# Kernel tuning notes

Hardware: AMD Instinct MI355X
Metric: run time of the kernel (lower is better)

The kernel has to match this reference:

```python
import jax, jax.numpy as jnp
import numpy as np

N_NODES = 100000
N_EDGES = 1_600_000
IN_CH = 64
HID = 128
OUT_CH = 2


def _glorot(key, shape):
    fan_in = shape[0]
    return jax.random.normal(key, shape, dtype=jnp.float32) / jnp.sqrt(jnp.float32(fan_in))


def setup_inputs() -> dict:
    key = jax.random.key(0)
    ks = jax.random.split(key, 10)
    x = jax.random.normal(ks[0], (N_NODES, IN_CH), dtype=jnp.float32)
    edge_index = jax.random.randint(ks[1], (2, N_EDGES), 0, N_NODES, dtype=jnp.int64)
    # SAGEConv layer 0: lin_l (neighbor, with bias) + lin_r (root)
    W_n0 = _glorot(ks[2], (IN_CH, HID))
    W_s0 = _glorot(ks[3], (IN_CH, HID))
    b0 = jnp.zeros((HID,), dtype=jnp.float32)
    # SAGEConv layer 1
    W_n1 = _glorot(ks[4], (HID, HID))
    W_s1 = _glorot(ks[5], (HID, HID))
    b1 = jnp.zeros((HID,), dtype=jnp.float32)
    # final fc
    fc_w = _glorot(ks[6], (HID, OUT_CH))
    fc_b = jnp.zeros((OUT_CH,), dtype=jnp.float32)
    return {"x": x, "edge_index": edge_index, "W_n0": W_n0, "W_s0": W_s0, "b0": b0,
            "W_n1": W_n1, "W_s1": W_s1, "b1": b1, "fc_w": fc_w, "fc_b": fc_b}


def _sage_conv(h, src, dst, W_n, W_s, b, num_nodes):
    # mean aggregation of source features onto destination nodes
    agg = jax.ops.segment_sum(h[src], dst, num_segments=num_nodes)  # [N, d]
    cnt = jax.ops.segment_sum(jnp.ones_like(dst, dtype=h.dtype), dst, num_segments=num_nodes)
    mean = agg / jnp.maximum(cnt, 1.0)[:, None]
    return mean @ W_n + h @ W_s + b


def reference(x, edge_index, W_n0, W_s0, b0, W_n1, W_s1, b1, fc_w, fc_b):
    src, dst = edge_index[0], edge_index[1]
    n = x.shape[0]
    h = jax.nn.relu(_sage_conv(x, src, dst, W_n0, W_s0, b0, n))  # dropout is identity in eval mode
    h = jax.nn.relu(_sage_conv(h, src, dst, W_n1, W_s1, b1, n))
    return h @ fc_w + fc_b
```

## Files before the change

kernel.cpp:

```cpp
#include <hip/hip_runtime.h>

#define N_NODES 100000
#define IN_CH 64
#define HID 128
#define NBUCK ((N_NODES + 511) >> 9)
#define NCB 256

typedef short short8 __attribute__((ext_vector_type(8)));
typedef float floatx4 __attribute__((ext_vector_type(4)));
typedef float floatx2 __attribute__((ext_vector_type(2)));

__device__ __forceinline__ unsigned short f2bf(float f) {
    unsigned u = __builtin_bit_cast(unsigned, f);
    u += 0x7fffu + ((u >> 16) & 1u);
    return (unsigned short)(u >> 16);
}

template <int K>
__device__ __forceinline__ void pack_dev(const float* __restrict__ Wn,
                                         const float* __restrict__ Ws,
                                         unsigned short* __restrict__ Bpack, int idx) {
    int s = idx >> 9;
    int rem = idx & 511;
    int t = rem >> 6;
    int lane = rem & 63;
    int quad = lane >> 4;
    int n = t * 16 + (lane & 15);
    unsigned short v[8];
#pragma unroll
    for (int j = 0; j < 8; ++j) {
        int k = s * 32 + quad * 8 + j;
        float w = (k < K) ? Wn[(size_t)k * HID + n] : Ws[(size_t)(k - K) * HID + n];
        v[j] = f2bf(w);
    }
    *(short8*)(Bpack + (size_t)idx * 8) = *(short8*)v;
}

__global__ __launch_bounds__(256) void histprep_kernel(const int* __restrict__ dst,
                                                       int* __restrict__ table, int E, int chunk,
                                                       const float* __restrict__ x,
                                                       unsigned short* __restrict__ x_bf,
                                                       unsigned char* __restrict__ x_f8,
                                                       const float* __restrict__ Wn0,
                                                       const float* __restrict__ Ws0,
                                                       unsigned short* __restrict__ Bpack0,
                                                       const float* __restrict__ Wn1,
                                                       const float* __restrict__ Ws1,
                                                       unsigned short* __restrict__ Bpack1,
                                                       int* __restrict__ scan_done, int n4) {
    int b = blockIdx.x;
    if (b < NCB) {
        if (b == 0 && threadIdx.x == 0) *scan_done = 0;
        __shared__ int h[NBUCK];
        for (int i = threadIdx.x; i < NBUCK; i += 256) h[i] = 0;
        __syncthreads();
        int e0 = b * chunk;
        int e1 = min(E, e0 + chunk);
        for (int e = e0 + threadIdx.x; e < e1; e += 256) atomicAdd(&h[dst[e] >> 9], 1);
        __syncthreads();
        for (int i = threadIdx.x; i < NBUCK; i += 256) table[i * NCB + b] = h[i];
    } else if (b < NCB + 8) {
        pack_dev<IN_CH>(Wn0, Ws0, Bpack0, (b - NCB) * 256 + threadIdx.x);
    } else if (b < NCB + 24) {
        pack_dev<HID>(Wn1, Ws1, Bpack1, (b - NCB - 8) * 256 + threadIdx.x);
    } else {
        int i = (b - NCB - 24) * 256 + threadIdx.x;
        if (i < n4) {
            float4 v = ((const float4*)x)[i];
            ushort4 o;
            o.x = f2bf(v.x); o.y = f2bf(v.y); o.z = f2bf(v.z); o.w = f2bf(v.w);
            ((ushort4*)x_bf)[i] = o;
            int p8 = __builtin_amdgcn_cvt_pk_fp8_f32(v.x, v.y, 0, false);
            p8 = __builtin_amdgcn_cvt_pk_fp8_f32(v.z, v.w, p8, true);
            ((unsigned*)x_f8)[i] = (unsigned)p8;
        }
    }
}

__global__ __launch_bounds__(256) void scan12_kernel(int* __restrict__ table,
                                                     int* __restrict__ tot,
                                                     int* __restrict__ bstart,
                                                     int* __restrict__ ptr,
                                                     int* __restrict__ scan_done, int E) {
    __shared__ int s[NCB];
    __shared__ int lastflag;
    int b = blockIdx.x, t = threadIdx.x;
    int c = table[b * NCB + t];
    s[t] = c;
    __syncthreads();
#pragma unroll
    for (int off = 1; off < NCB; off <<= 1) {
        int v = (t >= off) ? s[t - off] : 0;
        __syncthreads();
        s[t] += v;
        __syncthreads();
    }
    table[b * NCB + t] = s[t] - c;
    if (t == NCB - 1) {
        __hip_atomic_store(&tot[b], s[t], __ATOMIC_RELAXED, __HIP_MEMORY_SCOPE_AGENT);
        int prev = __hip_atomic_fetch_add(scan_done, 1, __ATOMIC_ACQ_REL, __HIP_MEMORY_SCOPE_AGENT);
        lastflag = (prev == NBUCK - 1);
    }
    __syncthreads();
    if (!lastflag) return;
    int v = (t < NBUCK) ? __hip_atomic_load(&tot[t], __ATOMIC_RELAXED, __HIP_MEMORY_SCOPE_AGENT) : 0;
    s[t] = v;
    __syncthreads();
#pragma unroll
    for (int off = 1; off < 256; off <<= 1) {
        int u = (t >= off) ? s[t - off] : 0;
        __syncthreads();
        s[t] += u;
        __syncthreads();
    }
    if (t < NBUCK) bstart[t] = s[t] - v;
    if (t == 0) {
        bstart[NBUCK] = E;
        ptr[N_NODES] = E;
    }
}

__global__ __launch_bounds__(256) void bin_kernel(const int* __restrict__ src,
                                                  const int* __restrict__ dst,
                                                  const int* __restrict__ table,
                                                  const int* __restrict__ bstart,
                                                  unsigned* __restrict__ binned, int E, int chunk) {
    __shared__ int cur[NBUCK];
    int blk = blockIdx.x;
    for (int i = threadIdx.x; i < NBUCK; i += 256) cur[i] = bstart[i] + table[i * NCB + blk];
    __syncthreads();
    int e0 = blk * chunk;
    int e1 = min(E, e0 + chunk);
    for (int e = e0 + threadIdx.x; e < e1; e += 256) {
        int d = dst[e];
        int b = d >> 9;
        int pos = atomicAdd(&cur[b], 1);
        binned[pos] = (unsigned)src[e] | ((unsigned)(d & 511) << 17);
    }
}

__global__ __launch_bounds__(256) void place_kernel(const unsigned* __restrict__ binned,
                                                    const int* __restrict__ bstart,
                                                    int* __restrict__ ptr,
                                                    int* __restrict__ sorted, int N) {
    __shared__ int deg[512];
    __shared__ int cur[512];
    __shared__ int ssum[256];
    int b = blockIdx.x, t = threadIdx.x;
    int start = bstart[b], end = bstart[b + 1];
    deg[t] = 0;
    deg[t + 256] = 0;
    __syncthreads();
    for (int i = start + t; i < end; i += 256) atomicAdd(&deg[binned[i] >> 17], 1);
    __syncthreads();
    int a = deg[2 * t], c = deg[2 * t + 1];
    int s2 = a + c;
    ssum[t] = s2;
    __syncthreads();
#pragma unroll
    for (int off = 1; off < 256; off <<= 1) {
        int u = (t >= off) ? ssum[t - off] : 0;
        __syncthreads();
        ssum[t] += u;
        __syncthreads();
    }
    int excl2 = ssum[t] - s2;
    cur[2 * t] = excl2;
    cur[2 * t + 1] = excl2 + a;
    int n0 = b * 512 + 2 * t;
    if (n0 < N) ptr[n0] = start + excl2;
    if (n0 + 1 < N) ptr[n0 + 1] = start + excl2 + a;
    __syncthreads();
    for (int i = start + t; i < end; i += 256) {
        unsigned p = binned[i];
        int dl = p >> 17;
        int pos = start + atomicAdd(&cur[dl], 1);
        sorted[pos] = (int)(p & 0x1FFFF);
    }
}

template <int C>
__global__ __launch_bounds__(256) void gather_mean_f8(const int* __restrict__ ptr,
                                                      const int* __restrict__ srcs,
                                                      const unsigned char* __restrict__ feat,
                                                      unsigned short* __restrict__ mean, int N) {
    constexpr int NA = C / 64;
    int w = (blockIdx.x * blockDim.x + threadIdx.x) >> 6;
    if (w >= N) return;
    int lane = threadIdx.x & 63;
    int g = lane >> 4;
    int l = lane & 15;
    int s0 = ptr[w], s1 = ptr[w + 1];
    int deg = s1 - s0;

    floatx2 acc2[2 * NA];
#pragma unroll
    for (int u = 0; u < 2 * NA; ++u) { acc2[u][0] = 0.0f; acc2[u][1] = 0.0f; }

    for (int jb = 0; jb < deg; jb += 64) {
        int rem = min(64, deg - jb);
        int idxreg = (jb + lane < deg) ? srcs[s0 + jb + lane] : 0;
        int fullend = rem & ~15;
        int o0 = 0;
        for (; o0 < fullend; o0 += 16) {
            uint v[4][NA];
#pragma unroll
            for (int q = 0; q < 4; ++q) {
                int idx = __shfl(idxreg, o0 + q * 4 + g);
                if (NA == 2) {
                    uint2 tt = *(const uint2*)(feat + (size_t)idx * C + l * 8);
                    v[q][0] = tt.x; v[q][1] = tt.y;
                } else {
                    v[q][0] = *(const unsigned*)(feat + (size_t)idx * C + l * 4);
                }
            }
#pragma unroll
            for (int q = 0; q < 4; ++q)
#pragma unroll
                for (int a = 0; a < NA; ++a) {
                    acc2[2 * a + 0] += __builtin_amdgcn_cvt_pk_f32_fp8(v[q][a], false);
                    acc2[2 * a + 1] += __builtin_amdgcn_cvt_pk_f32_fp8(v[q][a], true);
                }
        }
        if (o0 < rem) {
            uint v[4][NA];
#pragma unroll
            for (int q = 0; q < 4; ++q) {
                int o = o0 + q * 4 + g;
                int idx = __shfl(idxreg, o);
#pragma unroll
                for (int a = 0; a < NA; ++a) v[q][a] = 0;
                if (o < rem) {
                    if (NA == 2) {
                        uint2 tt = *(const uint2*)(feat + (size_t)idx * C + l * 8);
                        v[q][0] = tt.x; v[q][1] = tt.y;
                    } else {
                        v[q][0] = *(const unsigned*)(feat + (size_t)idx * C + l * 4);
                    }
                }
            }
#pragma unroll
            for (int q = 0; q < 4; ++q)
#pragma unroll
                for (int a = 0; a < NA; ++a) {
                    acc2[2 * a + 0] += __builtin_amdgcn_cvt_pk_f32_fp8(v[q][a], false);
                    acc2[2 * a + 1] += __builtin_amdgcn_cvt_pk_f32_fp8(v[q][a], true);
                }
        }
    }
#pragma unroll
    for (int m = 16; m < 64; m <<= 1) {
#pragma unroll
        for (int u = 0; u < 2 * NA; ++u) {
            acc2[u][0] += __shfl_xor(acc2[u][0], m, 64);
            acc2[u][1] += __shfl_xor(acc2[u][1], m, 64);
        }
    }
    if (g == 0) {
        float inv = (deg > 0) ? 1.0f / (float)deg : 0.0f;
        unsigned short o[4 * NA];
#pragma unroll
        for (int u = 0; u < 2 * NA; ++u) {
            o[2 * u + 0] = f2bf(acc2[u][0] * inv);
            o[2 * u + 1] = f2bf(acc2[u][1] * inv);
        }
        if (NA == 2) *(uint4*)(mean + (size_t)w * C + l * 8) = *(const uint4*)o;
        else *(uint2*)(mean + (size_t)w * C + l * 4) = *(const uint2*)o;
    }
}

template <int KT, bool FUSE_FC>
__global__ __launch_bounds__(256) void sage_gemm_mfma(const unsigned short* __restrict__ meanb,
                                                      const unsigned short* __restrict__ hb,
                                                      const unsigned short* __restrict__ Bpack,
                                                      const float* __restrict__ bias,
                                                      const float* __restrict__ fcw,
                                                      const float* __restrict__ fcb,
                                                      unsigned short* __restrict__ outb,
                                                      unsigned char* __restrict__ out8,
                                                      float* __restrict__ outf, int N) {
    constexpr int KH = KT / 2;
    constexpr int LDA = KT + 8;
    __shared__ unsigned short As[64 * LDA];
    const int t = threadIdx.x;
    const int row0 = blockIdx.x * 64;

    constexpr int SEGS = KT / 8;
    for (int c = t; c < 64 * SEGS; c += 256) {
        int r = c / SEGS, seg = c % SEGS;
        int rsrc = row0 + r;
        if (rsrc >= N) rsrc = N - 1;
        const unsigned short* srcp = (seg < SEGS / 2)
                                         ? meanb + (size_t)rsrc * KH + seg * 8
                                         : hb + (size_t)rsrc * KH + (seg - SEGS / 2) * 8;
        *(uint4*)&As[r * LDA + seg * 8] = *(const uint4*)srcp;
    }
    __syncthreads();

    const int lane = t & 63;
    const int wave = t >> 6;
    const int quad = lane >> 4;
    const int lo = lane & 15;

    floatx4 acc[8];
#pragma unroll
    for (int i = 0; i < 8; ++i)
#pragma unroll
        for (int r = 0; r < 4; ++r) acc[i][r] = 0.0f;

    const unsigned short* abase = &As[(wave * 16 + lo) * LDA + quad * 8];
#pragma unroll
    for (int s = 0; s < KT / 32; ++s) {
        short8 a = *(const short8*)(abase + s * 32);
        const short8* bp = (const short8*)Bpack + (size_t)(s * 8) * 64 + lane;
#pragma unroll
        for (int tt = 0; tt < 8; ++tt) {
            short8 b = bp[tt * 64];
            acc[tt] = __builtin_amdgcn_mfma_f32_16x16x32_bf16(a, b, acc[tt], 0, 0, 0);
        }
    }

    if (!FUSE_FC) {
        __syncthreads();
#pragma unroll
        for (int tt = 0; tt < 8; ++tt) {
            int col = tt * 16 + lo;
            float bv = bias[col];
#pragma unroll
            for (int r = 0; r < 4; ++r) {
                int rl = wave * 16 + quad * 4 + r;
                As[rl * LDA + col] = f2bf(fmaxf(acc[tt][r] + bv, 0.0f));
            }
        }
        __syncthreads();
        for (int i = t; i < 64 * (HID / 8); i += 256) {
            int r = i >> 4, ch = i & 15;
            int row = row0 + r;
            if (row < N)
                *(uint4*)(outb + (size_t)row * HID + ch * 8) = *(const uint4*)&As[r * LDA + ch * 8];
        }
        __syncthreads();
        unsigned char* As8 = (unsigned char*)As;
#pragma unroll
        for (int tt = 0; tt < 8; ++tt) {
            int col = tt * 16 + lo;
            float bv = bias[col];
#pragma unroll
            for (int r = 0; r < 4; ++r) {
                int rl = wave * 16 + quad * 4 + r;
                float v = fmaxf(acc[tt][r] + bv, 0.0f);
                int p8 = __builtin_amdgcn_cvt_pk_fp8_f32(v, v, 0, false);
                As8[rl * (LDA * 2) + col] = (unsigned char)(p8 & 0xff);
            }
        }
        __syncthreads();
        for (int i = t; i < 64 * (HID / 16); i += 256) {
            int r = i >> 3, ch = i & 7;
            int row = row0 + r;
            if (row < N)
                *(uint4*)(out8 + (size_t)row * HID + ch * 16) =
                    *(const uint4*)&As8[r * (LDA * 2) + ch * 16];
        }
    } else {
        float o0[4] = {}, o1[4] = {};
#pragma unroll
        for (int tt = 0; tt < 8; ++tt) {
            int col = tt * 16 + lo;
            float bv = bias[col];
            float w0 = fcw[col * 2 + 0];
            float w1 = fcw[col * 2 + 1];
#pragma unroll
            for (int r = 0; r < 4; ++r) {
                float v = fmaxf(acc[tt][r] + bv, 0.0f);
                o0[r] += v * w0;
                o1[r] += v * w1;
            }
        }
#pragma unroll
        for (int r = 0; r < 4; ++r) {
#pragma unroll
            for (int m = 8; m >= 1; m >>= 1) {
                o0[r] += __shfl_xor(o0[r], m, 16);
                o1[r] += __shfl_xor(o1[r], m, 16);
            }
        }
        if (lo == 0) {
#pragma unroll
            for (int r = 0; r < 4; ++r) {
                int row = row0 + wave * 16 + quad * 4 + r;
                if (row < N) {
                    outf[(size_t)row * 2 + 0] = o0[r] + fcb[0];
                    outf[(size_t)row * 2 + 1] = o1[r] + fcb[1];
                }
            }
        }
    }
}

extern "C" void kernel_launch(void* const* d_in, const int* in_sizes, int n_in,
                              void* d_out, int out_size, void* d_ws, size_t ws_size,
                              hipStream_t stream) {
    const float* x   = (const float*)d_in[0];
    const int*   ei  = (const int*)d_in[1];
    const float* Wn0 = (const float*)d_in[2];
    const float* Ws0 = (const float*)d_in[3];
    const float* b0  = (const float*)d_in[4];
    const float* Wn1 = (const float*)d_in[5];
    const float* Ws1 = (const float*)d_in[6];
    const float* b1  = (const float*)d_in[7];
    const float* fcw = (const float*)d_in[8];
    const float* fcb = (const float*)d_in[9];
    float* out = (float*)d_out;

    const int E = in_sizes[1] / 2;
    const int* src = ei;
    const int* dst = ei + E;
    const int N = N_NODES;
    const int chunk = (E + NCB - 1) / NCB;

    char* ws = (char*)d_ws;
    size_t off = 0;
    int* table  = (int*)(ws + off); off += (size_t)NBUCK * NCB * 4;
    int* tot    = (int*)(ws + off); off += 4096;
    int* bstart = (int*)(ws + off); off += 4096;
    int* scan_done = (int*)(ws + off); off += 256;
    int* ptr    = (int*)(ws + off); off += (size_t)(N + 1) * 4 + 60; off &= ~(size_t)63;
    unsigned* binned = (unsigned*)(ws + off); off += (size_t)E * 4;
    int* sorted = (int*)(ws + off); off += (size_t)E * 4;
    off = (off + 255) & ~(size_t)255;
    unsigned short* x_bf   = (unsigned short*)(ws + off); off += (size_t)N * IN_CH * 2;
    unsigned short* mean0  = (unsigned short*)(ws + off); off += (size_t)N * IN_CH * 2;
    unsigned short* h1_bf  = (unsigned short*)(ws + off); off += (size_t)N * HID * 2;
    unsigned short* mean1  = (unsigned short*)(ws + off); off += (size_t)N * HID * 2;
    unsigned char*  h1_f8  = (unsigned char*)(ws + off);  off += (size_t)N * HID;
    unsigned char*  x_f8   = (unsigned char*)(ws + off);  off += (size_t)N * IN_CH;
    off = (off + 255) & ~(size_t)255;
    unsigned short* Bpack0 = (unsigned short*)(ws + off); off += (size_t)(2 * IN_CH / 32) * 8 * 64 * 8 * 2;
    unsigned short* Bpack1 = (unsigned short*)(ws + off); off += (size_t)(2 * HID / 32) * 8 * 64 * 8 * 2;

    {
        int n4 = N * IN_CH / 4;
        int nblk = NCB + 24 + (n4 + 255) / 256;
        histprep_kernel<<<nblk, 256, 0, stream>>>(dst, table, E, chunk, x, x_bf, x_f8,
                                                  Wn0, Ws0, Bpack0, Wn1, Ws1, Bpack1,
                                                  scan_done, n4);
    }
    scan12_kernel<<<NBUCK, 256, 0, stream>>>(table, tot, bstart, ptr, scan_done, E);
    bin_kernel<<<NCB, 256, 0, stream>>>(src, dst, table, bstart, binned, E, chunk);
    place_kernel<<<NBUCK, 256, 0, stream>>>(binned, bstart, ptr, sorted, N);

    gather_mean_f8<IN_CH><<<(N * 64 + 255) / 256, 256, 0, stream>>>(ptr, sorted, x_f8, mean0, N);
    sage_gemm_mfma<2 * IN_CH, false><<<(N + 63) / 64, 256, 0, stream>>>(
        mean0, x_bf, Bpack0, b0, nullptr, nullptr, h1_bf, h1_f8, nullptr, N);

    gather_mean_f8<HID><<<(N * 64 + 255) / 256, 256, 0, stream>>>(ptr, sorted, h1_f8, mean1, N);
    sage_gemm_mfma<2 * HID, true><<<(N + 63) / 64, 256, 0, stream>>>(
        mean1, h1_bf, Bpack1, b1, fcw, fcb, nullptr, nullptr, out, N);
}
```

Baseline: 253.3 us.

## Fuse neighbor mean gather into SAGE MFMA GEMM kernel, drop mean buffers

Merges the per-node mean-gather kernel with the following MFMA GEMM. Each 64-row block now has every wave gather 16 destination rows serially and write the bf16 means straight into the shared-memory A tile, so the mean0/mean1 global round trip and two launches go away. Bounds clamps are added to bin/place and to gather indices, and degree is capped at 1024. The trade-off is less parallelism during the gather: one wave handles 16 rows in sequence instead of one wave per node, which may hurt latency hiding. The degree cap could also change results for very high-degree nodes.

Result: slower. 281.8 us (+11.2%).

```diff
diff --git a/kernel.cpp b/kernel.cpp
--- a/kernel.cpp
+++ b/kernel.cpp
@@ -135,23 +135,26 @@
         int d = dst[e];
         int b = d >> 9;
         int pos = atomicAdd(&cur[b], 1);
-        binned[pos] = (unsigned)src[e] | ((unsigned)(d & 511) << 17);
+        if ((unsigned)pos < (unsigned)E)
+            binned[pos] = (unsigned)src[e] | ((unsigned)(d & 511) << 17);
     }
 }
 
 __global__ __launch_bounds__(256) void place_kernel(const unsigned* __restrict__ binned,
                                                     const int* __restrict__ bstart,
                                                     int* __restrict__ ptr,
-                                                    int* __restrict__ sorted, int N) {
+                                                    int* __restrict__ sorted, int N, int E) {
     __shared__ int deg[512];
     __shared__ int cur[512];
     __shared__ int ssum[256];
     int b = blockIdx.x, t = threadIdx.x;
     int start = bstart[b], end = bstart[b + 1];
+    start = max(0, min(start, E));
+    end = max(start, min(end, E));
     deg[t] = 0;
     deg[t + 256] = 0;
     __syncthreads();
-    for (int i = start + t; i < end; i += 256) atomicAdd(&deg[binned[i] >> 17], 1);
+    for (int i = start + t; i < end; i += 256) atomicAdd(&deg[(binned[i] >> 17) & 511], 1);
     __syncthreads();
     int a = deg[2 * t], c = deg[2 * t + 1];
     int s2 = a + c;
@@ -173,64 +176,71 @@
     __syncthreads();
     for (int i = start + t; i < end; i += 256) {
         unsigned p = binned[i];
-        int dl = p >> 17;
+        int dl = (p >> 17) & 511;
         int pos = start + atomicAdd(&cur[dl], 1);
-        sorted[pos] = (int)(p & 0x1FFFF);
-    }
-}
-
-template <int C>
-__global__ __launch_bounds__(256) void gather_mean_f8(const int* __restrict__ ptr,
-                                                      const int* __restrict__ srcs,
-                                                      const unsigned char* __restrict__ feat,
-                                                      unsigned short* __restrict__ mean, int N) {
+        if ((unsigned)pos < (unsigned)E) sorted[pos] = (int)(p & 0x1FFFF);
+    }
+}
+
+template <int C, bool FUSE_FC>
+__global__ __launch_bounds__(256) void sage_fused(const int* __restrict__ ptr,
+                                                  const int* __restrict__ srcs,
+                                                  const unsigned char* __restrict__ feat,
+                                                  const unsigned short* __restrict__ hb,
+                                                  const unsigned short* __restrict__ Bpack,
+                                                  const float* __restrict__ bias,
+                                                  const float* __restrict__ fcw,
+                                                  const float* __restrict__ fcb,
+                                                  unsigned short* __restrict__ outb,
+                                                  unsigned char* __restrict__ out8,
+                                                  float* __restrict__ outf, int N, int E) {
+    constexpr int KT = 2 * C;
+    constexpr int KH = C;
     constexpr int NA = C / 64;
-    int w = (blockIdx.x * blockDim.x + threadIdx.x) >> 6;
-    if (w >= N) return;
-    int lane = threadIdx.x & 63;
-    int g = lane >> 4;
-    int l = lane & 15;
-    int s0 = ptr[w], s1 = ptr[w + 1];
-    int deg = s1 - s0;
-
-    floatx2 acc2[2 * NA];
-#pragma unroll
-    for (int u = 0; u < 2 * NA; ++u) { acc2[u][0] = 0.0f; acc2[u][1] = 0.0f; }
-
-    for (int jb = 0; jb < deg; jb += 64) {
-        int rem = min(64, deg - jb);
-        int idxreg = (jb + lane < deg) ? srcs[s0 + jb + lane] : 0;
-        int fullend = rem & ~15;
-        int o0 = 0;
-        for (; o0 < fullend; o0 += 16) {
-            uint v[4][NA];
-#pragma unroll
-            for (int q = 0; q < 4; ++q) {
-                int idx = __shfl(idxreg, o0 + q * 4 + g);
-                if (NA == 2) {
-                    uint2 tt = *(const uint2*)(feat + (size_t)idx * C + l * 8);
-                    v[q][0] = tt.x; v[q][1] = tt.y;
-                } else {
-                    v[q][0] = *(const unsigned*)(feat + (size_t)idx * C + l * 4);
-                }
-            }
-#pragma unroll
-            for (int q = 0; q < 4; ++q)
-#pragma unroll
-                for (int a = 0; a < NA; ++a) {
-                    acc2[2 * a + 0] += __builtin_amdgcn_cvt_pk_f32_fp8(v[q][a], false);
-                    acc2[2 * a + 1] += __builtin_amdgcn_cvt_pk_f32_fp8(v[q][a], true);
-                }
-        }
-        if (o0 < rem) {
-            uint v[4][NA];
-#pragma unroll
-            for (int q = 0; q < 4; ++q) {
-                int o = o0 + q * 4 + g;
-                int idx = __shfl(idxreg, o);
-#pragma unroll
-                for (int a = 0; a < NA; ++a) v[q][a] = 0;
-                if (o < rem) {
+    constexpr int LDA = KT + 8;
+    __shared__ unsigned short As[64 * LDA];
+    const int t = threadIdx.x;
+    const int row0 = blockIdx.x * 64;
+    const int lane = t & 63;
+    const int wave = t >> 6;
+    const int g = lane >> 4;
+    const int l = lane & 15;
+
+    constexpr int SEGH = KH / 8;
+    constexpr int NSELF = (16 * SEGH) / 64;
+    uint4 selfreg[NSELF];
+#pragma unroll
+    for (int u = 0; u < NSELF; ++u) {
+        int c = lane + u * 64;
+        int rsrc = row0 + wave * 16 + c / SEGH;
+        if (rsrc >= N) rsrc = N - 1;
+        selfreg[u] = *(const uint4*)(hb + (size_t)rsrc * KH + (c % SEGH) * 8);
+    }
+
+#pragma unroll 1
+    for (int i = 0; i < 16; ++i) {
+        const int r = wave * 16 + i;
+        const int w = row0 + r;
+        if (w >= N) break;
+        int s0 = ptr[w], s1 = ptr[w + 1];
+        s0 = max(0, min(s0, E));
+        s1 = max(s0, min(s1, E));
+        const int deg = min(s1 - s0, 1024);
+
+        floatx2 acc2[2 * NA];
+#pragma unroll
+        for (int u = 0; u < 2 * NA; ++u) { acc2[u][0] = 0.0f; acc2[u][1] = 0.0f; }
+
+        for (int jb = 0; jb < deg; jb += 64) {
+            int rem = min(64, deg - jb);
+            int idxreg = (jb + lane < deg) ? srcs[s0 + jb + lane] : 0;
+            int fullend = rem & ~15;
+            int o0 = 0;
+            for (; o0 < fullend; o0 += 16) {
+                uint v[4][NA];
+#pragma unroll
+                for (int q = 0; q < 4; ++q) {
+                    int idx = min(__shfl(idxreg, o0 + q * 4 + g), N_NODES - 1);
                     if (NA == 2) {
                         uint2 tt = *(const uint2*)(feat + (size_t)idx * C + l * 8);
                         v[q][0] = tt.x; v[q][1] = tt.y;
@@ -238,69 +248,67 @@
                         v[q][0] = *(const unsigned*)(feat + (size_t)idx * C + l * 4);
                     }
                 }
-            }
-#pragma unroll
-            for (int q = 0; q < 4; ++q)
-#pragma unroll
-                for (int a = 0; a < NA; ++a) {
-                    acc2[2 * a + 0] += __builtin_amdgcn_cvt_pk_f32_fp8(v[q][a], false);
-                    acc2[2 * a + 1] += __builtin_amdgcn_cvt_pk_f32_fp8(v[q][a], true);
+#pragma unroll
+                for (int q = 0; q < 4; ++q)
+#pragma unroll
+                    for (int a = 0; a < NA; ++a) {
+                        acc2[2 * a + 0] += __builtin_amdgcn_cvt_pk_f32_fp8(v[q][a], false);
+                        acc2[2 * a + 1] += __builtin_amdgcn_cvt_pk_f32_fp8(v[q][a], true);
+                    }
+            }
+            if (o0 < rem) {
+                uint v[4][NA];
+#pragma unroll
+                for (int q = 0; q < 4; ++q) {
+                    int o = o0 + q * 4 + g;
+                    int idx = min(__shfl(idxreg, o), N_NODES - 1);
+#pragma unroll
+                    for (int a = 0; a < NA; ++a) v[q][a] = 0;
+                    if (o < rem) {
+                        if (NA == 2) {
+                            uint2 tt = *(const uint2*)(feat + (size_t)idx * C + l * 8);
+                            v[q][0] = tt.x; v[q][1] = tt.y;
+                        } else {
+                            v[q][0] = *(const unsigned*)(feat + (size_t)idx * C + l * 4);
+                        }
+                    }
                 }
-        }
-    }
-#pragma unroll
-    for (int m = 16; m < 64; m <<= 1) {
-#pragma unroll
-        for (int u = 0; u < 2 * NA; ++u) {
-            acc2[u][0] += __shfl_xor(acc2[u][0], m, 64);
-            acc2[u][1] += __shfl_xor(acc2[u][1], m, 64);
-        }
-    }
-    if (g == 0) {
-        float inv = (deg > 0) ? 1.0f / (float)deg : 0.0f;
-        unsigned short o[4 * NA];
-#pragma unroll
-        for (int u = 0; u < 2 * NA; ++u) {
-            o[2 * u + 0] = f2bf(acc2[u][0] * inv);
-            o[2 * u + 1] = f2bf(acc2[u][1] * inv);
-        }
-        if (NA == 2) *(uint4*)(mean + (size_t)w * C + l * 8) = *(const uint4*)o;
-        else *(uint2*)(mean + (size_t)w * C + l * 4) = *(const uint2*)o;
-    }
-}
-
-template <int KT, bool FUSE_FC>
-__global__ __launch_bounds__(256) void sage_gemm_mfma(const unsigned short* __restrict__ meanb,
-                                                      const unsigned short* __restrict__ hb,
-                                                      const unsigned short* __restrict__ Bpack,
-                                                      const float* __restrict__ bias,
-                                                      const float* __restrict__ fcw,
-                                                      const float* __restrict__ fcb,
-                                                      unsigned short* __restrict__ outb,
-                                                      unsigned char* __restrict__ out8,
-                                                      float* __restrict__ outf, int N) {
-    constexpr int KH = KT / 2;
-    constexpr int LDA = KT + 8;
-    __shared__ unsigned short As[64 * LDA];
-    const int t = threadIdx.x;
-    const int row0 = blockIdx.x * 64;
-
-    constexpr int SEGS = KT / 8;
-    for (int c = t; c < 64 * SEGS; c += 256) {
-        int r = c / SEGS, seg = c % SEGS;
-        int rsrc = row0 + r;
-        if (rsrc >= N) rsrc = N - 1;
-        const unsigned short* srcp = (seg < SEGS / 2)
-                                         ? meanb + (size_t)rsrc * KH + seg * 8
-                                         : hb + (size_t)rsrc * KH + (seg - SEGS / 2) * 8;
-        *(uint4*)&As[r * LDA + seg * 8] = *(const uint4*)srcp;
-    }
-    __syncthreads();
-
-    const int lane = t & 63;
-    const int wave = t >> 6;
-    const int quad = lane >> 4;
-    const int lo = lane & 15;
+#pragma unroll
+                for (int q = 0; q < 4; ++q)
+#pragma unroll
+                    for (int a = 0; a < NA; ++a) {
+                        acc2[2 * a + 0] += __builtin_amdgcn_cvt_pk_f32_fp8(v[q][a], false);
+                        acc2[2 * a + 1] += __builtin_amdgcn_cvt_pk_f32_fp8(v[q][a], true);
+                    }
+            }
+        }
+#pragma unroll
+        for (int m = 16; m < 64; m <<= 1)
+#pragma unroll
+            for (int u = 0; u < 2 * NA; ++u) {
+                acc2[u][0] += __shfl_xor(acc2[u][0], m, 64);
+                acc2[u][1] += __shfl_xor(acc2[u][1], m, 64);
+            }
+        if (g == 0) {
+            float inv = (deg > 0) ? 1.0f / (float)deg : 0.0f;
+            unsigned short o[4 * NA];
+#pragma unroll
+            for (int u = 0; u < 2 * NA; ++u) {
+                o[2 * u + 0] = f2bf(acc2[u][0] * inv);
+                o[2 * u + 1] = f2bf(acc2[u][1] * inv);
+            }
+            if (NA == 2) *(uint4*)&As[r * LDA + l * 8] = *(const uint4*)o;
+            else *(uint2*)&As[r * LDA + l * 4] = *(const uint2*)o;
+        }
+    }
+
+#pragma unroll
+    for (int u = 0; u < NSELF; ++u) {
+        int c = lane + u * 64;
+        int r = wave * 16 + c / SEGH;
+        *(uint4*)&As[r * LDA + KH + (c % SEGH) * 8] = selfreg[u];
+    }
+    __syncthreads();
 
     floatx4 acc[8];
 #pragma unroll
@@ -308,7 +316,7 @@
 #pragma unroll
         for (int r = 0; r < 4; ++r) acc[i][r] = 0.0f;
 
-    const unsigned short* abase = &As[(wave * 16 + lo) * LDA + quad * 8];
+    const unsigned short* abase = &As[(wave * 16 + l) * LDA + g * 8];
 #pragma unroll
     for (int s = 0; s < KT / 32; ++s) {
         short8 a = *(const short8*)(abase + s * 32);
@@ -324,11 +332,11 @@
         __syncthreads();
 #pragma unroll
         for (int tt = 0; tt < 8; ++tt) {
-            int col = tt * 16 + lo;
+            int col = tt * 16 + l;
             float bv = bias[col];
 #pragma unroll
             for (int r = 0; r < 4; ++r) {
-                int rl = wave * 16 + quad * 4 + r;
+                int rl = wave * 16 + g * 4 + r;
                 As[rl * LDA + col] = f2bf(fmaxf(acc[tt][r] + bv, 0.0f));
             }
         }
@@ -343,11 +351,11 @@
         unsigned char* As8 = (unsigned char*)As;
 #pragma unroll
         for (int tt = 0; tt < 8; ++tt) {
-            int col = tt * 16 + lo;
+            int col = tt * 16 + l;
             float bv = bias[col];
 #pragma unroll
             for (int r = 0; r < 4; ++r) {
-                int rl = wave * 16 + quad * 4 + r;
+                int rl = wave * 16 + g * 4 + r;
                 float v = fmaxf(acc[tt][r] + bv, 0.0f);
                 int p8 = __builtin_amdgcn_cvt_pk_fp8_f32(v, v, 0, false);
                 As8[rl * (LDA * 2) + col] = (unsigned char)(p8 & 0xff);
@@ -365,7 +373,7 @@
         float o0[4] = {}, o1[4] = {};
 #pragma unroll
         for (int tt = 0; tt < 8; ++tt) {
-            int col = tt * 16 + lo;
+            int col = tt * 16 + l;
             float bv = bias[col];
             float w0 = fcw[col * 2 + 0];
             float w1 = fcw[col * 2 + 1];
@@ -384,10 +392,10 @@
                 o1[r] += __shfl_xor(o1[r], m, 16);
             }
         }
-        if (lo == 0) {
+        if (l == 0) {
 #pragma unroll
             for (int r = 0; r < 4; ++r) {
-                int row = row0 + wave * 16 + quad * 4 + r;
+                int row = row0 + wave * 16 + g * 4 + r;
                 if (row < N) {
                     outf[(size_t)row * 2 + 0] = o0[r] + fcb[0];
                     outf[(size_t)row * 2 + 1] = o1[r] + fcb[1];
@@ -429,9 +437,7 @@
     int* sorted = (int*)(ws + off); off += (size_t)E * 4;
     off = (off + 255) & ~(size_t)255;
     unsigned short* x_bf   = (unsigned short*)(ws + off); off += (size_t)N * IN_CH * 2;
-    unsigned short* mean0  = (unsigned short*)(ws + off); off += (size_t)N * IN_CH * 2;
     unsigned short* h1_bf  = (unsigned short*)(ws + off); off += (size_t)N * HID * 2;
-    unsigned short* mean1  = (unsigned short*)(ws + off); off += (size_t)N * HID * 2;
     unsigned char*  h1_f8  = (unsigned char*)(ws + off);  off += (size_t)N * HID;
     unsigned char*  x_f8   = (unsigned char*)(ws + off);  off += (size_t)N * IN_CH;
     off = (off + 255) & ~(size_t)255;
@@ -447,13 +453,11 @@
     }
     scan12_kernel<<<NBUCK, 256, 0, stream>>>(table, tot, bstart, ptr, scan_done, E);
     bin_kernel<<<NCB, 256, 0, stream>>>(src, dst, table, bstart, binned, E, chunk);
-    place_kernel<<<NBUCK, 256, 0, stream>>>(binned, bstart, ptr, sorted, N);
-
-    gather_mean_f8<IN_CH><<<(N * 64 + 255) / 256, 256, 0, stream>>>(ptr, sorted, x_f8, mean0, N);
-    sage_gemm_mfma<2 * IN_CH, false><<<(N + 63) / 64, 256, 0, stream>>>(
-        mean0, x_bf, Bpack0, b0, nullptr, nullptr, h1_bf, h1_f8, nullptr, N);
-
-    gather_mean_f8<HID><<<(N * 64 + 255) / 256, 256, 0, stream>>>(ptr, sorted, h1_f8, mean1, N);
-    sage_gemm_mfma<2 * HID, true><<<(N + 63) / 64, 256, 0, stream>>>(
-        mean1, h1_bf, Bpack1, b1, fcw, fcb, nullptr, nullptr, out, N);
-}
+    place_kernel<<<NBUCK, 256, 0, stream>>>(binned, bstart, ptr, sorted, N, E);
+
+    const int sblk = (N + 63) / 64;
+    sage_fused<IN_CH, false><<<sblk, 256, 0, stream>>>(
+        ptr, sorted, x_f8, x_bf, Bpack0, b0, nullptr, nullptr, h1_bf, h1_f8, nullptr, N, E);
+    sage_fused<HID, true><<<sblk, 256, 0, stream>>>(
+        ptr, sorted, h1_f8, h1_bf, Bpack1, b1, fcw, fcb, nullptr, nullptr, out, N, E);
+}
```
